# Kernel tuning notes

Measured on AMD Instinct MI355X. Metric: run time of the kernel, lower is better.

## Reference

```python
import jax, jax.numpy as jnp
import numpy as np

L, T, B, D, H, DQK, DV, FF = 4, 1024, 4, 1024, 16, 64, 64, 4096
EPS = 1e-6


def setup_inputs() -> dict:
    key = jax.random.key(0)
    ks = jax.random.split(key, 11)
    s = 0.02
    f32 = jnp.float32
    return {
        "x": jax.random.normal(ks[0], (T, B, D), f32),
        "mask": jnp.ones((B, T), bool),
        "Wk": jax.random.normal(ks[1], (L, D, H * DQK), f32) * s,
        "bk": jnp.zeros((L, H * DQK), f32),
        "Wq": jax.random.normal(ks[2], (L, D, H * DQK), f32) * s,
        "bq": jnp.zeros((L, H * DQK), f32),
        "Wv": jax.random.normal(ks[3], (L, D, H * DV), f32) * s,
        "bv": jnp.zeros((L, H * DV), f32),
        "W1": jax.random.normal(ks[4], (L, D, FF), f32) * s,
        "b1": jnp.zeros((L, FF), f32),
        "W2": jax.random.normal(ks[5], (L, FF, D), f32) * s,
        "b2": jnp.zeros((L, D), f32),
    }


def _resnorm(x, fx):
    # residual + (x - mean) / (std + eps); torch.std is unbiased (ddof=1)
    y = x + fx
    mu = y.mean(-1, keepdims=True)
    sd = y.std(-1, keepdims=True, ddof=1)
    return (y - mu) / (sd + EPS)


def _ff(x, W1, b1, W2, b2):
    # Feedforward default puts ReLU after every linear layer, including the last
    h = jax.nn.relu(x @ W1 + b1)
    return jax.nn.relu(h @ W2 + b2)


def _attn(x, mask, Wk, bk, Wq, bq, Wv, bv):
    # x: (T, B, D); mask: (B, T)
    k = (x @ Wk + bk).reshape(T, B, H, DQK)
    q = (x @ Wq + bq).reshape(T, B, H, DQK)
    # kern[b,h,i,j] = <key_i, query_j> / sqrt(D)   (note: scaled by model dim D)
    kern = jnp.einsum('ibhj,kbhj->bhik', k, q) / np.sqrt(D)
    kern = jnp.where(mask[:, None, None, :], kern, -jnp.inf)
    A = jax.nn.softmax(kern, axis=-1)  # softmax over query axis (as in source)
    v = (x @ Wv + bv).reshape(T, B, H, DV)
    out = jnp.einsum('bhij,jbhk->ibhk', A, v)  # (T, B, H, DV)
    return out.reshape(T, B, H * DV)


def reference(x, mask, Wk, bk, Wq, bq, Wv, bv, W1, b1, W2, b2):
    for l in range(L):
        z = _resnorm(x, _ff(x, W1[l], b1[l], W2[l], b2[l]))
        x = _resnorm(z, _attn(z, mask, Wk[l], bk[l], Wq[l], bq[l], Wv[l], bv[l]))
    return x
```

## Files before the change

### kernel.cpp

```cpp
#include <hip/hip_runtime.h>
#include <cstdint>
#include <cstddef>

#define TT    1024
#define DD    1024
#define FFD   4096
#define NLAYER 4
#define MROWS 4096

typedef __bf16 bf16;
typedef __bf16 bf16x8 __attribute__((ext_vector_type(8)));
typedef __bf16 bf16x4v __attribute__((ext_vector_type(4)));
typedef float  f32x4  __attribute__((ext_vector_type(4)));

__device__ __forceinline__ bf16 f2b(float f) { return (bf16)f; }

typedef __attribute__((address_space(3))) unsigned int lds_u32;
typedef __attribute__((address_space(1))) const unsigned int g_u32;
__device__ __forceinline__ void gl_lds16(const bf16* g, bf16* l) {
    __builtin_amdgcn_global_load_lds((g_u32*)g, (lds_u32*)l, 16, 0, 0);
}

__global__ __launch_bounds__(256) void cvt_k(const float* __restrict__ src,
                                             bf16* __restrict__ dst) {
    const int i = blockIdx.x * 256 + threadIdx.x;
    f32x4 v = *(const f32x4*)(src + (size_t)i * 4);
    bf16x4v o;
#pragma unroll
    for (int u = 0; u < 4; ++u) o[u] = f2b(v[u]);
    *(bf16x4v*)(dst + (size_t)i * 4) = o;
}

__device__ __forceinline__ void tr_tile(const float* __restrict__ src,
                                        bf16* __restrict__ dst, int R, int C,
                                        int bx, int by, int t) {
    __shared__ bf16 tile[32][33];
    const int tx = t & 31, ty = (t >> 5) * 4;
    const int c0 = bx * 32, r0 = by * 32;
#pragma unroll
    for (int u = 0; u < 4; ++u)
        tile[ty + u][tx] = f2b(src[(size_t)(r0 + ty + u) * C + c0 + tx]);
    __syncthreads();
#pragma unroll
    for (int u = 0; u < 4; ++u)
        dst[(size_t)(c0 + ty + u) * R + r0 + tx] = tile[tx][ty + u];
}

__global__ __launch_bounds__(256) void prep_k(const float* __restrict__ W1,
                                              const float* __restrict__ W2,
                                              const float* __restrict__ Wk,
                                              const float* __restrict__ Wq,
                                              const float* __restrict__ Wv,
                                              const float* __restrict__ bkp,
                                              const float* __restrict__ bqp,
                                              const float* __restrict__ bvp,
                                              bf16* __restrict__ w1t,
                                              bf16* __restrict__ w2t,
                                              bf16* __restrict__ kqvt,
                                              float* __restrict__ bcat) {
    const int id = blockIdx.x, t = threadIdx.x;
    if (id < 4096) {
        tr_tile(W1, w1t, 1024, 4096, id & 127, id >> 7, t);
    } else if (id < 8192) {
        const int r = id - 4096;
        tr_tile(W2, w2t, 4096, 1024, r & 31, r >> 5, t);
    } else if (id < 9216) {
        const int r = id - 8192;
        tr_tile(Wk, kqvt, 1024, 1024, r & 31, r >> 5, t);
    } else if (id < 10240) {
        const int r = id - 9216;
        tr_tile(Wq, kqvt + 1048576, 1024, 1024, r & 31, r >> 5, t);
    } else if (id < 11264) {
        const int r = id - 10240;
        tr_tile(Wv, kqvt + 2097152, 1024, 1024, r & 31, r >> 5, t);
    } else {
        const int i = (id - 11264) * 256 + t;
        bcat[i] = (i < 1024) ? bkp[i] : (i < 2048 ? bqp[i - 1024] : bvp[i - 2048]);
    }
}

__global__ __launch_bounds__(256) void vtrans_k(const bf16* __restrict__ src,
                                                bf16* __restrict__ dst) {
    __shared__ bf16 tile[32][33];
    const int t  = threadIdx.x;
    const int tx = t & 31, ty = (t >> 5) * 4;
    const int bh = blockIdx.z, tt = blockIdx.y * 32, dv0 = blockIdx.x * 32;
    const int b = bh >> 4, h = bh & 15;
#pragma unroll
    for (int u = 0; u < 4; ++u)
        tile[ty + u][tx] = src[(size_t)((tt + ty + u) * 4 + b) * 3072 + h * 64 + dv0 + tx];
    __syncthreads();
#pragma unroll
    for (int u = 0; u < 4; ++u)
        dst[(size_t)(bh * 64 + dv0 + ty + u) * 1024 + tt + tx] = tile[tx][ty + u];
}

template <bool RELU, int BN>
__global__ __launch_bounds__(256) void gemm_bt(const bf16* __restrict__ A, int lda,
                                               const bf16* __restrict__ Bt, int ldb,
                                               const float* __restrict__ bias,
                                               bf16* __restrict__ C, int ldc, int K) {
    constexpr int WC = (BN == 128) ? 2 : 1;
    constexpr int MW = 128 / (4 / WC);
    constexpr int NW = BN / WC;
    constexpr int MI = MW / 16;
    constexpr int NI = NW / 16;
    constexpr int NB = BN / 32;
    __shared__ bf16 As[128 * 64];
    __shared__ bf16 Bs[BN * 64];
    const int t = threadIdx.x;
    const int w = t >> 6, lane = t & 63, l15 = lane & 15, qd = lane >> 4;
    const int m0 = blockIdx.y * 128, n0 = blockIdx.x * BN;
    const int wr = (w / WC) * MW, wc = (w % WC) * NW;
    const int srow = lane >> 3, scol = ((lane & 7) ^ srow) * 8;
    const int sx = (l15 & 7) << 3;
    f32x4 acc[MI][NI] = {};
    for (int k0 = 0; k0 < K; k0 += 64) {
#pragma unroll
        for (int i = 0; i < 4; ++i) {
            const int r0 = (w * 4 + i) * 8;
            gl_lds16(A + (size_t)(m0 + r0 + srow) * lda + k0 + scol, As + r0 * 64 + lane * 8);
        }
#pragma unroll
        for (int i = 0; i < NB; ++i) {
            const int r0 = (w * NB + i) * 8;
            gl_lds16(Bt + (size_t)(n0 + r0 + srow) * ldb + k0 + scol, Bs + r0 * 64 + lane * 8);
        }
        __syncthreads();
#pragma unroll
        for (int kk = 0; kk < 64; kk += 32) {
            bf16x8 af[MI], bfr[NI];
#pragma unroll
            for (int i = 0; i < MI; ++i)
                af[i] = *(const bf16x8*)(As + (wr + i * 16 + l15) * 64 + ((kk + qd * 8) ^ sx));
#pragma unroll
            for (int j = 0; j < NI; ++j)
                bfr[j] = *(const bf16x8*)(Bs + (wc + j * 16 + l15) * 64 + ((kk + qd * 8) ^ sx));
#pragma unroll
            for (int i = 0; i < MI; ++i)
#pragma unroll
                for (int j = 0; j < NI; ++j)
                    acc[i][j] = __builtin_amdgcn_mfma_f32_16x16x32_bf16(af[i], bfr[j], acc[i][j], 0, 0, 0);
        }
        __syncthreads();
    }
#pragma unroll
    for (int j = 0; j < NI; ++j) {
        const int col = n0 + wc + j * 16 + l15;
        const float bz = bias[col];
#pragma unroll
        for (int i = 0; i < MI; ++i) {
            const int row = m0 + wr + i * 16 + qd * 4;
#pragma unroll
            for (int p = 0; p < 4; ++p) {
                float c = acc[i][j][p] + bz;
                if (RELU) c = fmaxf(c, 0.f);
                C[(size_t)(row + p) * ldc + col] = f2b(c);
            }
        }
    }
}

__device__ __forceinline__ float block_sum(float s, float* red, int w, int lane) {
#pragma unroll
    for (int off = 32; off >= 1; off >>= 1) s += __shfl_xor(s, off, 64);
    if (lane == 0) red[w] = s;
    __syncthreads();
    return red[0] + red[1] + red[2] + red[3];
}

template <bool OUT_F32>
__global__ __launch_bounds__(256) void resnorm_k(const bf16* __restrict__ x,
                                                 const bf16* __restrict__ fx,
                                                 void* __restrict__ outv) {
    __shared__ float red1[4], red2[4];
    const int t = threadIdx.x, w = t >> 6, lane = t & 63;
    const size_t base = (size_t)blockIdx.x * DD + t * 4;
    bf16x4v xv = *(const bf16x4v*)(x + base);
    bf16x4v fv = *(const bf16x4v*)(fx + base);
    float y[4], s = 0.f;
#pragma unroll
    for (int u = 0; u < 4; ++u) { y[u] = (float)xv[u] + (float)fv[u]; s += y[u]; }
    s = block_sum(s, red1, w, lane);
    const float mu = s * (1.f / DD);
    float v = 0.f;
#pragma unroll
    for (int u = 0; u < 4; ++u) { const float d = y[u] - mu; v += d * d; }
    v = block_sum(v, red2, w, lane);
    const float sd = sqrtf(v * (1.f / (DD - 1)));
    const float ri = 1.f / (sd + 1e-6f);
    if (OUT_F32) {
        f32x4 ov;
#pragma unroll
        for (int u = 0; u < 4; ++u) ov[u] = (y[u] - mu) * ri;
        *(f32x4*)((float*)outv + base) = ov;
    } else {
        bf16x4v ov;
#pragma unroll
        for (int u = 0; u < 4; ++u) ov[u] = f2b((y[u] - mu) * ri);
        *(bf16x4v*)((bf16*)outv + base) = ov;
    }
}

__global__ __launch_bounds__(256, 2) void attn_k(const bf16* __restrict__ kq,
                                                 const bf16* __restrict__ vt,
                                                 bf16* __restrict__ out) {
    __shared__ bf16 smem[17408 + 9216 + 8704];
    bf16* PlK = smem;
    bf16* Qt  = smem + 17408;
    bf16* Vts = smem + 17408 + 9216;
    const int t = threadIdx.x;
    const int w = t >> 6, lane = t & 63, l15 = lane & 15, qd = lane >> 4;
    const int i0 = blockIdx.x * 128, bh = blockIdx.y, b = bh >> 4, h = bh & 15;
    const size_t kbase = (size_t)b * 3072 + h * 64;
    const int sr = t >> 3, sc = (t & 7) * 8;
    const int vr = t >> 2, vc = (t & 3) * 32;
    const float SC = 0.03125f;

#pragma unroll
    for (int ch = 0; ch < 4; ++ch) {
        const int r = ch * 32 + sr;
        *(bf16x8*)(PlK + r * 72 + sc) =
            *(const bf16x8*)(kq + (size_t)(i0 + r) * 12288 + kbase + sc);
    }
    __syncthreads();
    bf16x8 kf[2][2];
#pragma unroll
    for (int i = 0; i < 2; ++i)
#pragma unroll
        for (int kx = 0; kx < 2; ++kx)
            kf[i][kx] = *(const bf16x8*)(PlK + (w * 32 + i * 16 + l15) * 72 + kx * 32 + qd * 8);
    bf16* Pl = PlK + w * 4352;

    f32x4 acc_o[2][4] = {};
    float lsum[2][4] = {};

    for (int j0 = 0; j0 < TT; j0 += 128) {
#pragma unroll
        for (int ch = 0; ch < 4; ++ch) {
            const int r = ch * 32 + sr;
            *(bf16x8*)(Qt + r * 72 + sc) =
                *(const bf16x8*)(kq + (size_t)(j0 + r) * 12288 + kbase + 1024 + sc);
        }
#pragma unroll
        for (int u = 0; u < 4; ++u)
            *(bf16x8*)(Vts + vr * 136 + vc + u * 8) =
                *(const bf16x8*)(vt + (size_t)(bh * 64 + vr) * 1024 + j0 + vc + u * 8);
        __syncthreads();

        f32x4 accs[2][8] = {};
#pragma unroll
        for (int kx = 0; kx < 2; ++kx) {
            bf16x8 bfr[8];
#pragma unroll
            for (int j = 0; j < 8; ++j)
                bfr[j] = *(const bf16x8*)(Qt + (j * 16 + l15) * 72 + kx * 32 + qd * 8);
#pragma unroll
            for (int i = 0; i < 2; ++i)
#pragma unroll
                for (int j = 0; j < 8; ++j)
                    accs[i][j] = __builtin_amdgcn_mfma_f32_16x16x32_bf16(kf[i][kx], bfr[j], accs[i][j], 0, 0, 0);
        }

#pragma unroll
        for (int i = 0; i < 2; ++i)
#pragma unroll
            for (int j = 0; j < 8; ++j)
#pragma unroll
                for (int p = 0; p < 4; ++p) {
                    const float pv = __expf(accs[i][j][p] * SC);
                    lsum[i][p] += pv;
                    Pl[(i * 16 + qd * 4 + p) * 136 + j * 16 + l15] = f2b(pv);
                }

#pragma unroll
        for (int kt = 0; kt < 4; ++kt) {
            bf16x8 pa[2], vb[4];
#pragma unroll
            for (int i = 0; i < 2; ++i)
                pa[i] = *(const bf16x8*)(Pl + (i * 16 + l15) * 136 + kt * 32 + qd * 8);
#pragma unroll
            for (int n = 0; n < 4; ++n)
                vb[n] = *(const bf16x8*)(Vts + (n * 16 + l15) * 136 + kt * 32 + qd * 8);
#pragma unroll
            for (int i = 0; i < 2; ++i)
#pragma unroll
                for (int n = 0; n < 4; ++n)
                    acc_o[i][n] = __builtin_amdgcn_mfma_f32_16x16x32_bf16(pa[i], vb[n], acc_o[i][n], 0, 0, 0);
        }
        __syncthreads();
    }

#pragma unroll
    for (int i = 0; i < 2; ++i)
#pragma unroll
        for (int p = 0; p < 4; ++p) {
            float s = lsum[i][p];
#pragma unroll
            for (int off = 1; off < 16; off <<= 1) s += __shfl_xor(s, off, 64);
            const float ri = 1.f / s;
            const int ig = i0 + w * 32 + i * 16 + qd * 4 + p;
#pragma unroll
            for (int n = 0; n < 4; ++n)
                out[(size_t)ig * 4096 + b * 1024 + h * 64 + n * 16 + l15] = f2b(acc_o[i][n][p] * ri);
        }
}

extern "C" void kernel_launch(void* const* d_in, const int* in_sizes, int n_in,
                              void* d_out, int out_size, void* d_ws, size_t ws_size,
                              hipStream_t stream) {
    const float* x_in = (const float*)d_in[0];
    const float* Wk = (const float*)d_in[2];
    const float* bk = (const float*)d_in[3];
    const float* Wq = (const float*)d_in[4];
    const float* bq = (const float*)d_in[5];
    const float* Wv = (const float*)d_in[6];
    const float* bv = (const float*)d_in[7];
    const float* W1 = (const float*)d_in[8];
    const float* b1 = (const float*)d_in[9];
    const float* W2 = (const float*)d_in[10];
    const float* b2 = (const float*)d_in[11];

    bf16* ws = (bf16*)d_ws;
    const size_t M1 = 1024 * 1024;
    bf16* w1t  = ws;
    bf16* w2t  = ws +  4 * M1;
    bf16* kqvt = ws +  8 * M1;
    bf16* vtb  = ws + 11 * M1;
    bf16* fbuf = ws + 15 * M1;
    bf16* zbuf = ws + 19 * M1;
    bf16* xb   = ws + 23 * M1;
    bf16* big  = ws + 27 * M1;
    float* bcat = (float*)(ws + 43 * M1);
    float* outp = (float*)d_out;

    cvt_k<<<dim3(MROWS * DD / 1024), 256, 0, stream>>>(x_in, xb);

    const bf16* xcur = xb;
    for (int l = 0; l < NLAYER; ++l) {
        prep_k<<<dim3(11276), 256, 0, stream>>>(
            W1 + (size_t)l * DD * FFD, W2 + (size_t)l * FFD * DD,
            Wk + (size_t)l * M1, Wq + (size_t)l * M1, Wv + (size_t)l * M1,
            bk + (size_t)l * DD, bq + (size_t)l * DD, bv + (size_t)l * DD,
            w1t, w2t, kqvt, bcat);
        gemm_bt<true, 128><<<dim3(FFD / 128, MROWS / 128), 256, 0, stream>>>(
            xcur, DD, w1t, DD, b1 + (size_t)l * FFD, big, FFD, DD);
        gemm_bt<true, 64><<<dim3(DD / 64, MROWS / 128), 256, 0, stream>>>(
            big, FFD, w2t, FFD, b2 + (size_t)l * DD, fbuf, DD, FFD);
        resnorm_k<false><<<dim3(MROWS), 256, 0, stream>>>(xcur, fbuf, zbuf);
        gemm_bt<false, 128><<<dim3(3072 / 128, MROWS / 128), 256, 0, stream>>>(
            zbuf, DD, kqvt, DD, bcat, big, 3072, DD);
        vtrans_k<<<dim3(2, 32, 64), 256, 0, stream>>>(big + 2048, vtb);
        attn_k<<<dim3(8, 64), 256, 0, stream>>>(big, vtb, fbuf);
        if (l == NLAYER - 1)
            resnorm_k<true><<<dim3(MROWS), 256, 0, stream>>>(zbuf, fbuf, outp);
        else
            resnorm_k<false><<<dim3(MROWS), 256, 0, stream>>>(zbuf, fbuf, xb);
        xcur = xb;
    }
}
```

Baseline: 1.030 ms.

## Double-buffer LDS in FFN down-projection GEMM and remap blocks across XCDs

Result: faster. 1.009 ms (-2.1%).

```diff
diff --git a/kernel.cpp b/kernel.cpp
--- a/kernel.cpp
+++ b/kernel.cpp
@@ -95,7 +95,7 @@
         dst[(size_t)(bh * 64 + dv0 + ty + u) * 1024 + tt + tx] = tile[tx][ty + u];
 }
 
-template <bool RELU, int BN>
+template <bool RELU, int BN, bool DBUF>
 __global__ __launch_bounds__(256) void gemm_bt(const bf16* __restrict__ A, int lda,
                                                const bf16* __restrict__ Bt, int ldb,
                                                const float* __restrict__ bias,
@@ -106,44 +106,76 @@
     constexpr int MI = MW / 16;
     constexpr int NI = NW / 16;
     constexpr int NB = BN / 32;
-    __shared__ bf16 As[128 * 64];
-    __shared__ bf16 Bs[BN * 64];
+    constexpr int NBUF = DBUF ? 2 : 1;
+    __shared__ bf16 As[NBUF][128 * 64];
+    __shared__ bf16 Bs[NBUF][BN * 64];
     const int t = threadIdx.x;
     const int w = t >> 6, lane = t & 63, l15 = lane & 15, qd = lane >> 4;
-    const int m0 = blockIdx.y * 128, n0 = blockIdx.x * BN;
+    int bid = blockIdx.y * gridDim.x + blockIdx.x;
+    {
+        const int q = (int)(gridDim.x * gridDim.y) >> 3;
+        bid = (bid & 7) * q + (bid >> 3);
+    }
+    const int bx = bid % (int)gridDim.x, by = bid / (int)gridDim.x;
+    const int m0 = by * 128, n0 = bx * BN;
     const int wr = (w / WC) * MW, wc = (w % WC) * NW;
     const int srow = lane >> 3, scol = ((lane & 7) ^ srow) * 8;
     const int sx = (l15 & 7) << 3;
     f32x4 acc[MI][NI] = {};
-    for (int k0 = 0; k0 < K; k0 += 64) {
+
+    auto stage = [&](int buf, int k0) {
 #pragma unroll
         for (int i = 0; i < 4; ++i) {
             const int r0 = (w * 4 + i) * 8;
-            gl_lds16(A + (size_t)(m0 + r0 + srow) * lda + k0 + scol, As + r0 * 64 + lane * 8);
+            gl_lds16(A + (size_t)(m0 + r0 + srow) * lda + k0 + scol,
+                     &As[buf][0] + r0 * 64 + lane * 8);
         }
 #pragma unroll
         for (int i = 0; i < NB; ++i) {
             const int r0 = (w * NB + i) * 8;
-            gl_lds16(Bt + (size_t)(n0 + r0 + srow) * ldb + k0 + scol, Bs + r0 * 64 + lane * 8);
-        }
-        __syncthreads();
+            gl_lds16(Bt + (size_t)(n0 + r0 + srow) * ldb + k0 + scol,
+                     &Bs[buf][0] + r0 * 64 + lane * 8);
+        }
+    };
+    auto compute = [&](int buf) {
 #pragma unroll
         for (int kk = 0; kk < 64; kk += 32) {
             bf16x8 af[MI], bfr[NI];
 #pragma unroll
             for (int i = 0; i < MI; ++i)
-                af[i] = *(const bf16x8*)(As + (wr + i * 16 + l15) * 64 + ((kk + qd * 8) ^ sx));
+                af[i] = *(const bf16x8*)(&As[buf][0] + (wr + i * 16 + l15) * 64 + ((kk + qd * 8) ^ sx));
 #pragma unroll
             for (int j = 0; j < NI; ++j)
-                bfr[j] = *(const bf16x8*)(Bs + (wc + j * 16 + l15) * 64 + ((kk + qd * 8) ^ sx));
+                bfr[j] = *(const bf16x8*)(&Bs[buf][0] + (wc + j * 16 + l15) * 64 + ((kk + qd * 8) ^ sx));
 #pragma unroll
             for (int i = 0; i < MI; ++i)
 #pragma unroll
                 for (int j = 0; j < NI; ++j)
                     acc[i][j] = __builtin_amdgcn_mfma_f32_16x16x32_bf16(af[i], bfr[j], acc[i][j], 0, 0, 0);
         }
+    };
+
+    if (DBUF) {
+        const int nt = K >> 6;
+        int cur = 0;
+        stage(0, 0);
         __syncthreads();
-    }
+        for (int it = 0; it < nt - 1; ++it) {
+            stage(cur ^ 1, (it + 1) << 6);
+            compute(cur);
+            __syncthreads();
+            cur ^= 1;
+        }
+        compute(cur);
+    } else {
+        for (int k0 = 0; k0 < K; k0 += 64) {
+            stage(0, k0);
+            __syncthreads();
+            compute(0);
+            __syncthreads();
+        }
+    }
+
 #pragma unroll
     for (int j = 0; j < NI; ++j) {
         const int col = n0 + wc + j * 16 + l15;
@@ -211,7 +243,9 @@
     bf16* Vts = smem + 17408 + 9216;
     const int t = threadIdx.x;
     const int w = t >> 6, lane = t & 63, l15 = lane & 15, qd = lane >> 4;
-    const int i0 = blockIdx.x * 128, bh = blockIdx.y, b = bh >> 4, h = bh & 15;
+    int bid = blockIdx.y * 8 + blockIdx.x;
+    bid = (bid & 7) * 64 + (bid >> 3);
+    const int i0 = (bid & 7) * 128, bh = bid >> 3, b = bh >> 4, h = bh & 15;
     const size_t kbase = (size_t)b * 3072 + h * 64;
     const int sr = t >> 3, sc = (t & 7) * 8;
     const int vr = t >> 2, vc = (t & 3) * 32;
@@ -343,12 +377,12 @@
             Wk + (size_t)l * M1, Wq + (size_t)l * M1, Wv + (size_t)l * M1,
             bk + (size_t)l * DD, bq + (size_t)l * DD, bv + (size_t)l * DD,
             w1t, w2t, kqvt, bcat);
-        gemm_bt<true, 128><<<dim3(FFD / 128, MROWS / 128), 256, 0, stream>>>(
+        gemm_bt<true, 128, false><<<dim3(FFD / 128, MROWS / 128), 256, 0, stream>>>(
             xcur, DD, w1t, DD, b1 + (size_t)l * FFD, big, FFD, DD);
-        gemm_bt<true, 64><<<dim3(DD / 64, MROWS / 128), 256, 0, stream>>>(
+        gemm_bt<true, 64, true><<<dim3(DD / 64, MROWS / 128), 256, 0, stream>>>(
             big, FFD, w2t, FFD, b2 + (size_t)l * DD, fbuf, DD, FFD);
         resnorm_k<false><<<dim3(MROWS), 256, 0, stream>>>(xcur, fbuf, zbuf);
-        gemm_bt<false, 128><<<dim3(3072 / 128, MROWS / 128), 256, 0, stream>>>(
+        gemm_bt<false, 128, false><<<dim3(3072 / 128, MROWS / 128), 256, 0, stream>>>(
             zbuf, DD, kqvt, DD, bcat, big, 3072, DD);
         vtrans_k<<<dim3(2, 32, 64), 256, 0, stream>>>(big + 2048, vtb);
         attn_k<<<dim3(8, 64), 256, 0, stream>>>(big, vtb, fbuf);
```
